# Kernel tuning notes

Hardware: AMD Instinct MI355X
Metric: run time of the kernel (lower is better)

Reference implementation:

```python
import jax, jax.numpy as jnp
import numpy as np

EPS = 1e-12
NEG_SLOPE = 0.2

def _normalize(x):
    # F.normalize(x, p=2, dim=1)
    n = jnp.sqrt(jnp.sum(x * x, axis=-1, keepdims=True))
    return x / jnp.maximum(n, EPS)

def setup_inputs() -> dict:
    key = jax.random.key(0)
    ks = jax.random.split(key, 10)
    n_users, n_items, n_entities = 100000, 50000, 200000
    n_rel, n_edges, n_inter, n_hops, d = 32, 2000000, 1000000, 2, 64
    return {
        "user_emb": jax.random.normal(ks[0], (n_users, d), jnp.float32) * 0.1,
        "entity_emb": jax.random.normal(ks[1], (n_entities, d), jnp.float32) * 0.1,
        "rel_weight": jax.random.normal(ks[2], (n_rel, d), jnp.float32) * 0.1,
        "gate1_w": jax.random.normal(ks[3], (n_hops, d, d), jnp.float32) * 0.1,
        "gate2_w": jax.random.normal(ks[4], (n_hops, d, d), jnp.float32) * 0.1,
        "head": jax.random.randint(ks[5], (n_edges,), 0, n_entities, jnp.int32),
        "tail": jax.random.randint(ks[6], (n_edges,), 0, n_entities, jnp.int32),
        "edge_type": jax.random.randint(ks[7], (n_edges,), 0, n_rel, jnp.int32),
        "mat_row": jax.random.randint(ks[8], (n_inter,), 0, n_users, jnp.int32),
        "mat_col": jax.random.randint(ks[9], (n_inter,), 0, n_items, jnp.int32),
    }

def reference(user_emb, entity_emb, rel_weight, gate1_w, gate2_w,
              head, tail, edge_type, mat_row, mat_col):
    n_users = user_emb.shape[0]
    n_entities = entity_emb.shape[0]
    n_items = 50000
    n_hops = gate1_w.shape[0]

    entity_res = entity_emb
    user_res = user_emb
    for i in range(n_hops):
        # KG aggregate: gather-scale-scatter over KG triples
        msg = entity_emb[tail] * rel_weight[edge_type]          # [E, d]
        entity_agg = jax.ops.segment_sum(msg, head, num_segments=n_entities)
        # CF aggregate: user -> item
        item_neigh = user_emb[mat_row] * rel_weight[0]          # [I, d]
        i_u_agg = jax.ops.segment_sum(item_neigh, mat_col, num_segments=n_items)
        # gated fusion of KG-side and CF-side item embeddings
        ea_items = entity_agg[:n_items]
        gi = jax.nn.leaky_relu(ea_items @ gate1_w[i].T + i_u_agg @ gate2_w[i].T,
                               negative_slope=NEG_SLOPE)
        item_fusion = gi * ea_items + (1.0 - gi) * i_u_agg
        # sparse mm with binary user-item matrix == segment_sum over rows
        user_agg = jax.ops.segment_sum(item_fusion[mat_col], mat_row,
                                       num_segments=n_users)
        entity_emb = jnp.concatenate([item_fusion, entity_agg[n_items:]], axis=0)
        entity_emb = _normalize(entity_emb)
        user_emb = _normalize(user_agg)
        entity_res = entity_res + entity_emb
        user_res = user_res + user_emb
    # concatenate outputs: [n_entities + n_users, d]
    return jnp.concatenate([entity_res, user_res], axis=0)
```

## Files before the change

kernel.cpp:

```cpp
#include <hip/hip_runtime.h>
#include <hip/hip_bf16.h>

#define D 64
#define N_USERS 100000
#define N_ITEMS 50000
#define N_ENT   200000
#define EPS 1e-12f
#define CHUNK 4096
#define NBINP 512
#define CAP   8192

typedef unsigned short u16;
typedef unsigned int u32;
typedef unsigned long long u64;

template<int MODE> struct Cfg;
template<> struct Cfg<0> { static constexpr int SHIFT = 9; static constexpr int NSEG = N_ENT;   };
template<> struct Cfg<1> { static constexpr int SHIFT = 7; static constexpr int NSEG = N_ITEMS; };
template<> struct Cfg<2> { static constexpr int SHIFT = 8; static constexpr int NSEG = N_USERS; };
template<int MODE> constexpr int nbin_of() {
  return (Cfg<MODE>::NSEG + (1 << Cfg<MODE>::SHIFT) - 1) >> Cfg<MODE>::SHIFT;
}

__device__ __forceinline__ float bf2f(u16 u) {
  return __uint_as_float(((unsigned)u) << 16);
}
__device__ __forceinline__ u16 f2bf(float f) {
  unsigned u = __float_as_uint(f);
  unsigned r = (u + 0x7FFFu + ((u >> 16) & 1u)) >> 16;
  return (u16)r;
}
__device__ __forceinline__ float wave_rsqnorm(float v) {
  float ss = v * v;
#pragma unroll
  for (int m = 1; m < 64; m <<= 1) ss += __shfl_xor(ss, m);
  return 1.f / fmaxf(sqrtf(ss), EPS);
}
__device__ __forceinline__ float bcast(float v, int k) {
  return __uint_as_float(__builtin_amdgcn_readlane(__float_as_uint(v), k));
}

__global__ __launch_bounds__(256) void init_embed(
    const float* __restrict__ ent, const float* __restrict__ usr,
    float* __restrict__ out_ent, float* __restrict__ out_usr,
    u16* __restrict__ ent_bf, u16* __restrict__ usr_bf) {
  int i = blockIdx.x * 256 + threadIdx.x;
  if (i < N_ENT * D) {
    float v = ent[i];
    out_ent[i] = v;
    ent_bf[i] = f2bf(v);
  }
  if (i < N_USERS * D) {
    float v = usr[i];
    out_usr[i] = v;
    usr_bf[i] = f2bf(v);
  }
}

__global__ __launch_bounds__(256) void scan_block(
    const int* __restrict__ in, int* __restrict__ out,
    int* __restrict__ bsum, int n) {
  __shared__ int sm[256];
  int tid = threadIdx.x;
  int i = blockIdx.x * 256 + tid;
  int v = (i < n) ? in[i] : 0;
  sm[tid] = v;
  __syncthreads();
  for (int ofs = 1; ofs < 256; ofs <<= 1) {
    int t = (tid >= ofs) ? sm[tid - ofs] : 0;
    __syncthreads();
    sm[tid] += t;
    __syncthreads();
  }
  if (i < n) out[i] = sm[tid] - v;
  if (tid == 255) bsum[blockIdx.x] = sm[255];
}

__global__ __launch_bounds__(1024) void scan_top(int* __restrict__ bsum, int nb) {
  __shared__ int sm[1024];
  int tid = threadIdx.x;
  int v = (tid < nb) ? bsum[tid] : 0;
  sm[tid] = v;
  __syncthreads();
  for (int ofs = 1; ofs < 1024; ofs <<= 1) {
    int t = (tid >= ofs) ? sm[tid - ofs] : 0;
    __syncthreads();
    sm[tid] += t;
    __syncthreads();
  }
  if (tid < nb) bsum[tid] = sm[tid] - v;
}

__global__ __launch_bounds__(256) void scan_addv(
    int* __restrict__ out, const int* __restrict__ bsum, int n) {
  int i = blockIdx.x * 256 + threadIdx.x;
  if (i < n) out[i] += bsum[blockIdx.x];
}

template<int MODE>
__global__ __launch_bounds__(256) void p1_hist(
    const int* __restrict__ keys, int n, int* __restrict__ bc, int nblk) {
  constexpr int SHIFT = Cfg<MODE>::SHIFT;
  constexpr int NBIN = nbin_of<MODE>();
  __shared__ int h[NBINP];
  int tid = threadIdx.x;
  h[tid] = 0; h[tid + 256] = 0;
  __syncthreads();
  int base = blockIdx.x * CHUNK;
  int end = min(base + CHUNK, n);
  for (int i = base + tid; i < end; i += 256)
    atomicAdd(&h[keys[i] >> SHIFT], 1);
  __syncthreads();
  for (int b = tid; b < NBIN; b += 256)
    bc[b * nblk + blockIdx.x] = h[b];
}

template<int MODE>
__global__ __launch_bounds__(256) void p1_scatter(
    const int* __restrict__ keys, const int* __restrict__ pa,
    const int* __restrict__ pb, int n, const int* __restrict__ sbc, int nblk,
    int2* __restrict__ out) {
  constexpr int SHIFT = Cfg<MODE>::SHIFT;
  constexpr int NBIN = nbin_of<MODE>();
  __shared__ int h[NBINP];
  __shared__ int cur[NBINP];
  __shared__ int bb[NBINP];
  __shared__ int2 staged[CHUNK];
  __shared__ int dstA[CHUNK];
  int tid = threadIdx.x;
  h[tid] = 0; h[tid + 256] = 0;
  __syncthreads();
  int base = blockIdx.x * CHUNK;
  int end = min(base + CHUNK, n);
  for (int i = base + tid; i < end; i += 256)
    atomicAdd(&h[keys[i] >> SHIFT], 1);
  __syncthreads();
  int o0 = h[tid], o1 = h[tid + 256];
  for (int ofs = 1; ofs < NBINP; ofs <<= 1) {
    int v0 = (tid >= ofs) ? h[tid - ofs] : 0;
    int v1 = (tid + 256 >= ofs) ? h[tid + 256 - ofs] : 0;
    __syncthreads();
    h[tid] += v0; h[tid + 256] += v1;
    __syncthreads();
  }
  int e0 = h[tid] - o0, e1 = h[tid + 256] - o1;
  cur[tid] = e0; cur[tid + 256] = e1;
  if (tid < NBIN)        bb[tid] = sbc[tid * nblk + blockIdx.x] - e0;
  if (tid + 256 < NBIN)  bb[tid + 256] = sbc[(tid + 256) * nblk + blockIdx.x] - e1;
  __syncthreads();
  for (int i = base + tid; i < end; i += 256) {
    int k = keys[i];
    int bin = k >> SHIFT;
    int payload;
    if constexpr (MODE == 0) payload = pa[i] | (pb[i] << 24);
    else                     payload = pa[i];
    int lp = atomicAdd(&cur[bin], 1);
    staged[lp] = make_int2(k, payload);
    dstA[lp] = bb[bin] + lp;
  }
  __syncthreads();
  int cnt = end - base;
  for (int t = tid; t < cnt; t += 256) out[dstA[t]] = staged[t];
}

template<int MODE>
__global__ __launch_bounds__(256) void p2_sort(
    const int2* __restrict__ binned, const int* __restrict__ sbc, int nblk,
    int n, int* __restrict__ vals, int* __restrict__ hids,
    int* __restrict__ off) {
  constexpr int SHIFT = Cfg<MODE>::SHIFT;
  constexpr int NSEG = Cfg<MODE>::NSEG;
  constexpr int SEGBIN = 1 << SHIFT;
  constexpr int NBIN = nbin_of<MODE>();
  __shared__ int h[NBINP];
  __shared__ int cur[NBINP];
  __shared__ int staged[CAP];
  int tid = threadIdx.x;
  int b = blockIdx.x;
  int start = sbc[b * nblk];
  int endp = (b == NBIN - 1) ? n : sbc[(b + 1) * nblk];
  int cnt = endp - start;
  h[tid] = 0; h[tid + 256] = 0;
  __syncthreads();
  int segbase = b << SHIFT;
  for (int t = tid; t < cnt; t += 256)
    atomicAdd(&h[binned[start + t].x - segbase], 1);
  __syncthreads();
  int o0 = h[tid], o1 = h[tid + 256];
  for (int ofs = 1; ofs < NBINP; ofs <<= 1) {
    int v0 = (tid >= ofs) ? h[tid - ofs] : 0;
    int v1 = (tid + 256 >= ofs) ? h[tid + 256 - ofs] : 0;
    __syncthreads();
    h[tid] += v0; h[tid + 256] += v1;
    __syncthreads();
  }
  int e0 = h[tid] - o0, e1 = h[tid + 256] - o1;
  if (tid < SEGBIN && segbase + tid < NSEG) off[segbase + tid] = start + e0;
  if (tid + 256 < SEGBIN && segbase + tid + 256 < NSEG)
    off[segbase + tid + 256] = start + e1;
  if (b == NBIN - 1 && tid == 0) off[NSEG] = n;
  cur[tid] = e0; cur[tid + 256] = e1;
  __syncthreads();
  if (cnt <= CAP) {
    for (int t = tid; t < cnt; t += 256) {
      int2 e = binned[start + t];
      int lp = atomicAdd(&cur[e.x - segbase], 1);
      staged[lp] = e.y;
      hids[start + lp] = e.x;
    }
    __syncthreads();
    for (int t = tid; t < cnt; t += 256) vals[start + t] = staged[t];
  } else {
    for (int t = tid; t < cnt; t += 256) {
      int2 e = binned[start + t];
      int lp = atomicAdd(&cur[e.x - segbase], 1);
      vals[start + lp] = e.y;
      hids[start + lp] = e.x;
    }
  }
}

template<bool REL>
__global__ __launch_bounds__(256) void edge_gather(
    const u16* __restrict__ tab, const float* __restrict__ relw,
    const int* __restrict__ pk, const int* __restrict__ hid,
    float* __restrict__ raw, int n) {
  __shared__ float lds_relw[REL ? 32 * D : 1];
  if (REL) {
    for (int i = threadIdx.x; i < 32 * D; i += 256) lds_relw[i] = relw[i];
    __syncthreads();
  }
  int win = blockIdx.x * 4 + (threadIdx.x >> 6);
  int S = win * 64;
  if (S >= n) return;
  int lane = threadIdx.x & 63;
  int cnt = min(64, n - S);
  int p  = (S + lane < n) ? pk[S + lane]  : 0;
  int hd = (S + lane < n) ? hid[S + lane] : -3;
  int hp = (S > 0) ? hid[S - 1] : -4;
  int hn = (S + 64 < n) ? hid[S + 64] : -5;
  int hnl = __shfl_down(hd, 1);
  if (lane == 63) hnl = hn;
  u64 real = __ballot(hd != hnl);
  if (cnt < 64) real &= (1ull << cnt) - 1ull;
  u64 emit = real | (1ull << (cnt - 1));
  bool start_in = (__shfl(hd, 0) != hp);
  float acc = 0.f;
  if (cnt == 64) {
    for (int base = 0; base < 64; base += 8) {
      u16 r[8]; int et[8];
#pragma unroll
      for (int k = 0; k < 8; ++k) {
        int q = __shfl(p, base + k);
        if (REL) {
          r[k] = tab[(size_t)(q & 0xFFFFFF) * D + lane];
          et[k] = ((unsigned)q) >> 24;
        } else {
          r[k] = tab[(size_t)q * D + lane];
        }
      }
#pragma unroll
      for (int k = 0; k < 8; ++k) {
        int j = base + k;
        float c = bf2f(r[k]);
        if (REL) c *= lds_relw[et[k] * D + lane];
        acc += c;
        if ((emit >> j) & 1ull) {
          int h = __shfl(hd, j);
          float* dst = raw + (size_t)h * D + lane;
          if (start_in && ((real >> j) & 1ull)) *dst = acc;
          else atomicAdd(dst, acc);
          acc = 0.f;
          start_in = true;
        }
      }
    }
  } else {
    for (int j = 0; j < cnt; ++j) {
      int q = __shfl(p, j);
      float c;
      if (REL) c = bf2f(tab[(size_t)(q & 0xFFFFFF) * D + lane]) *
                   lds_relw[(((unsigned)q) >> 24) * D + lane];
      else     c = bf2f(tab[(size_t)q * D + lane]);
      acc += c;
      if ((emit >> j) & 1ull) {
        int h = __shfl(hd, j);
        float* dst = raw + (size_t)h * D + lane;
        if (start_in && ((real >> j) & 1ull)) *dst = acc;
        else atomicAdd(dst, acc);
        acc = 0.f;
        start_in = true;
      }
    }
  }
}

__global__ __launch_bounds__(256) void fin_rows(
    const float* __restrict__ raw, u16* __restrict__ out_bf,
    float* __restrict__ res, int row0, int nrows) {
  int r = blockIdx.x * 4 + (threadIdx.x >> 6);
  if (r >= nrows) return;
  int row = row0 + r;
  int lane = threadIdx.x & 63;
  size_t o = (size_t)row * D + lane;
  float v = raw[o];
  float nv = v * wave_rsqnorm(v);
  out_bf[o] = f2bf(nv);
  res[o] += nv;
}

__global__ __launch_bounds__(256) void fuse_items(
    const float* __restrict__ ent_raw, const float* __restrict__ iu,
    const float* __restrict__ relw,
    const float* __restrict__ g1, const float* __restrict__ g2,
    u16* __restrict__ fus_bf, u16* __restrict__ ent_bf,
    float* __restrict__ res) {
  __shared__ float G1[D][D + 1];
  __shared__ float G2[D][D + 1];
  for (int i = threadIdx.x; i < D * D; i += 256) {
    G1[i >> 6][i & 63] = g1[i];
    G2[i >> 6][i & 63] = g2[i];
  }
  __syncthreads();
  int row = blockIdx.x * 4 + (threadIdx.x >> 6);
  if (row >= N_ITEMS) return;
  int lane = threadIdx.x & 63;
  size_t o = (size_t)row * D + lane;
  float eav = ent_raw[o];
  float uv = iu[o] * relw[lane];
  float s1 = 0.f, s2 = 0.f;
#pragma unroll
  for (int k = 0; k < D; ++k) {
    s1 += bcast(eav, k) * G1[lane][k];
    s2 += bcast(uv, k) * G2[lane][k];
  }
  float s = s1 + s2;
  float gi = s > 0.f ? s : 0.2f * s;
  float fus = gi * eav + (1.f - gi) * uv;
  fus_bf[o] = f2bf(fus);
  float nv = fus * wave_rsqnorm(fus);
  ent_bf[o] = f2bf(nv);
  res[o] += nv;
}

template<int MODE>
static void run_sort(const int* keys, const int* pa, const int* pb, int n,
                     int2* binned, int* vals, int* hids, int* off, int* bc,
                     int* bsum, hipStream_t stream) {
  constexpr int NBIN = nbin_of<MODE>();
  int nblk = (n + CHUNK - 1) / CHUNK;
  int len = NBIN * nblk;
  p1_hist<MODE><<<nblk, 256, 0, stream>>>(keys, n, bc, nblk);
  int nbs = (len + 255) / 256;
  scan_block<<<nbs, 256, 0, stream>>>(bc, bc, bsum, len);
  scan_top<<<1, 1024, 0, stream>>>(bsum, nbs);
  scan_addv<<<nbs, 256, 0, stream>>>(bc, bsum, len);
  p1_scatter<MODE><<<nblk, 256, 0, stream>>>(keys, pa, pb, n, bc, nblk, binned);
  p2_sort<MODE><<<NBIN, 256, 0, stream>>>(binned, bc, nblk, n, vals, hids, off);
}

extern "C" void kernel_launch(void* const* d_in, const int* in_sizes, int n_in,
                              void* d_out, int out_size, void* d_ws, size_t ws_size,
                              hipStream_t stream) {
  const float* user_emb = (const float*)d_in[0];
  const float* ent_emb  = (const float*)d_in[1];
  const float* relw     = (const float*)d_in[2];
  const float* g1       = (const float*)d_in[3];
  const float* g2       = (const float*)d_in[4];
  const int*   head     = (const int*)d_in[5];
  const int*   tail     = (const int*)d_in[6];
  const int*   etype    = (const int*)d_in[7];
  const int*   mrow     = (const int*)d_in[8];
  const int*   mcol     = (const int*)d_in[9];

  const int n_edges = in_sizes[5];
  const int n_inter = in_sizes[8];
  const int n_hops  = in_sizes[3] / (D * D);

  u16* ent_bf = (u16*)d_ws;
  u16* usr_bf = ent_bf + (size_t)N_ENT * D;
  u16* fus_bf = usr_bf + (size_t)N_USERS * D;
  float* ent_raw = (float*)(fus_bf + (size_t)N_ITEMS * D);
  float* usr_raw = ent_raw + (size_t)N_ENT * D;
  float* iu      = usr_raw;
  int* ip = (int*)(usr_raw + (size_t)N_USERS * D);
  int* o_head = ip;   ip += N_ENT + 1;
  int* o_col  = ip;   ip += N_ITEMS + 1;
  int* o_row  = ip;   ip += N_USERS + 1;
  int* pk_head = ip;  ip += n_edges;
  int* hid_h   = ip;  ip += n_edges;
  int* vr_col  = ip;  ip += n_inter;
  int* hid_c   = ip;  ip += n_inter;
  int* vc_row  = ip;  ip += n_inter;
  int* hid_r   = ip;  ip += n_inter;
  int* bc      = ip;  ip += 391 * ((n_edges + CHUNK - 1) / CHUNK) + 64;
  int* bsum    = ip;  ip += 1024;

  float* out_ent = (float*)d_out;
  float* out_usr = out_ent + (size_t)N_ENT * D;

  int2* bin_head = (int2*)d_out;
  int2* bin_col  = bin_head + n_edges;
  int2* bin_row  = bin_col + n_inter;

  run_sort<0>(head, tail, etype, n_edges, bin_head, pk_head, hid_h, o_head,
              bc, bsum, stream);
  run_sort<1>(mcol, mrow, nullptr, n_inter, bin_col, vr_col, hid_c, o_col,
              bc, bsum, stream);
  run_sort<2>(mrow, mcol, nullptr, n_inter, bin_row, vc_row, hid_r, o_row,
              bc, bsum, stream);

  init_embed<<<(N_ENT * D + 255) / 256, 256, 0, stream>>>(
      ent_emb, user_emb, out_ent, out_usr, ent_bf, usr_bf);

  const int nwin_kg = (n_edges + 63) / 64;
  const int nwin_in = (n_inter + 63) / 64;

  for (int i = 0; i < n_hops; ++i) {
    hipMemsetAsync(ent_raw, 0, (size_t)N_ENT * D * sizeof(float), stream);
    hipMemsetAsync(iu, 0, (size_t)N_ITEMS * D * sizeof(float), stream);

    edge_gather<true><<<(nwin_kg + 3) / 4, 256, 0, stream>>>(
        ent_bf, relw, pk_head, hid_h, ent_raw, n_edges);

    edge_gather<false><<<(nwin_in + 3) / 4, 256, 0, stream>>>(
        usr_bf, nullptr, vr_col, hid_c, iu, n_inter);

    fuse_items<<<(N_ITEMS + 3) / 4, 256, 0, stream>>>(
        ent_raw, iu, relw, g1 + (size_t)i * D * D, g2 + (size_t)i * D * D,
        fus_bf, ent_bf, out_ent);

    fin_rows<<<(N_ENT - N_ITEMS + 3) / 4, 256, 0, stream>>>(
        ent_raw, ent_bf, out_ent, N_ITEMS, N_ENT - N_ITEMS);

    hipMemsetAsync(usr_raw, 0, (size_t)N_USERS * D * sizeof(float), stream);
    edge_gather<false><<<(nwin_in + 3) / 4, 256, 0, stream>>>(
        fus_bf, nullptr, vc_row, hid_r, usr_raw, n_inter);

    fin_rows<<<(N_USERS + 3) / 4, 256, 0, stream>>>(
        usr_raw, usr_bf, out_usr, 0, N_USERS);
  }
}
```

Baseline: 588.8 us.

## Streamline sort binning and defer residual accumulation to one final pass

The preprocessing sort now builds global bin totals with atomics and has each block claim its bin slots atomically. This replaces the per-block histogram matrix and its three-kernel scan, and drops the segment offset writes. The item-fusion and entity-normalize kernels are merged into one launch, and the two per-hop memsets become one. The per-hop fp32 residual read-modify-write is removed: each hop's normalized embeddings go to ping-pong bf16 tables, and a single final_combine kernel sums them with the original fp32 inputs. The trade-off is that the residual terms are now summed from bf16-rounded values, and the order of elements within each bin depends on atomic timing.

```diff
diff --git a/kernel.cpp b/kernel.cpp
--- a/kernel.cpp
+++ b/kernel.cpp
@@ -7,6 +7,8 @@
 #define N_ENT   200000
 #define EPS 1e-12f
 #define CHUNK 4096
+#define HCHUNK 16384
+#define NBIN  391
 #define NBINP 512
 #define CAP   8192
 
@@ -18,9 +20,6 @@
 template<> struct Cfg<0> { static constexpr int SHIFT = 9; static constexpr int NSEG = N_ENT;   };
 template<> struct Cfg<1> { static constexpr int SHIFT = 7; static constexpr int NSEG = N_ITEMS; };
 template<> struct Cfg<2> { static constexpr int SHIFT = 8; static constexpr int NSEG = N_USERS; };
-template<int MODE> constexpr int nbin_of() {
-  return (Cfg<MODE>::NSEG + (1 << Cfg<MODE>::SHIFT) - 1) >> Cfg<MODE>::SHIFT;
-}
 
 __device__ __forceinline__ float bf2f(u16 u) {
   return __uint_as_float(((unsigned)u) << 16);
@@ -40,145 +39,104 @@
   return __uint_as_float(__builtin_amdgcn_readlane(__float_as_uint(v), k));
 }
 
-__global__ __launch_bounds__(256) void init_embed(
+__global__ __launch_bounds__(256) void conv_embed(
     const float* __restrict__ ent, const float* __restrict__ usr,
-    float* __restrict__ out_ent, float* __restrict__ out_usr,
     u16* __restrict__ ent_bf, u16* __restrict__ usr_bf) {
   int i = blockIdx.x * 256 + threadIdx.x;
-  if (i < N_ENT * D) {
-    float v = ent[i];
-    out_ent[i] = v;
-    ent_bf[i] = f2bf(v);
-  }
-  if (i < N_USERS * D) {
-    float v = usr[i];
-    out_usr[i] = v;
-    usr_bf[i] = f2bf(v);
-  }
-}
-
-__global__ __launch_bounds__(256) void scan_block(
-    const int* __restrict__ in, int* __restrict__ out,
-    int* __restrict__ bsum, int n) {
-  __shared__ int sm[256];
-  int tid = threadIdx.x;
-  int i = blockIdx.x * 256 + tid;
-  int v = (i < n) ? in[i] : 0;
-  sm[tid] = v;
-  __syncthreads();
-  for (int ofs = 1; ofs < 256; ofs <<= 1) {
-    int t = (tid >= ofs) ? sm[tid - ofs] : 0;
-    __syncthreads();
-    sm[tid] += t;
-    __syncthreads();
-  }
-  if (i < n) out[i] = sm[tid] - v;
-  if (tid == 255) bsum[blockIdx.x] = sm[255];
-}
-
-__global__ __launch_bounds__(1024) void scan_top(int* __restrict__ bsum, int nb) {
-  __shared__ int sm[1024];
-  int tid = threadIdx.x;
-  int v = (tid < nb) ? bsum[tid] : 0;
-  sm[tid] = v;
-  __syncthreads();
-  for (int ofs = 1; ofs < 1024; ofs <<= 1) {
-    int t = (tid >= ofs) ? sm[tid - ofs] : 0;
-    __syncthreads();
-    sm[tid] += t;
-    __syncthreads();
-  }
-  if (tid < nb) bsum[tid] = sm[tid] - v;
-}
-
-__global__ __launch_bounds__(256) void scan_addv(
-    int* __restrict__ out, const int* __restrict__ bsum, int n) {
-  int i = blockIdx.x * 256 + threadIdx.x;
-  if (i < n) out[i] += bsum[blockIdx.x];
-}
-
-template<int MODE>
-__global__ __launch_bounds__(256) void p1_hist(
-    const int* __restrict__ keys, int n, int* __restrict__ bc, int nblk) {
-  constexpr int SHIFT = Cfg<MODE>::SHIFT;
-  constexpr int NBIN = nbin_of<MODE>();
+  if (i < N_ENT * D) ent_bf[i] = f2bf(ent[i]);
+  if (i < N_USERS * D) usr_bf[i] = f2bf(usr[i]);
+}
+
+__global__ __launch_bounds__(256) void hist_tot(
+    const int* __restrict__ keys, int n, int shift, int* __restrict__ tot) {
   __shared__ int h[NBINP];
   int tid = threadIdx.x;
   h[tid] = 0; h[tid + 256] = 0;
   __syncthreads();
+  int base = blockIdx.x * HCHUNK;
+  int end = min(base + HCHUNK, n);
+  for (int i = base + tid; i < end; i += 256)
+    atomicAdd(&h[keys[i] >> shift], 1);
+  __syncthreads();
+  for (int b = tid; b < NBIN; b += 256)
+    if (h[b]) atomicAdd(&tot[b], h[b]);
+}
+
+__global__ __launch_bounds__(512) void scan_bases(
+    const int* __restrict__ tot, int* __restrict__ bases,
+    int* __restrict__ cur, int n0, int n1, int n2) {
+  __shared__ int sm[512];
+  int tid = threadIdx.x;
+  for (int s = 0; s < 3; ++s) {
+    int tn = (s == 0) ? n0 : ((s == 1) ? n1 : n2);
+    int v = (tid < NBIN) ? tot[s * 392 + tid] : 0;
+    __syncthreads();
+    sm[tid] = v;
+    __syncthreads();
+    for (int ofs = 1; ofs < 512; ofs <<= 1) {
+      int t = (tid >= ofs) ? sm[tid - ofs] : 0;
+      __syncthreads();
+      sm[tid] += t;
+      __syncthreads();
+    }
+    if (tid < NBIN) {
+      int b = sm[tid] - v;
+      bases[s * 392 + tid] = b;
+      cur[s * 392 + tid] = b;
+    }
+    if (tid == 0) bases[s * 392 + NBIN] = tn;
+  }
+}
+
+template<int MODE>
+__global__ __launch_bounds__(256) void p1_direct(
+    const int* __restrict__ keys, const int* __restrict__ pa,
+    const int* __restrict__ pb, int n, int* __restrict__ cur,
+    int2* __restrict__ out) {
+  constexpr int SHIFT = Cfg<MODE>::SHIFT;
+  __shared__ int lkeys[CHUNK];
+  __shared__ int h[NBINP];
+  __shared__ int bb[NBINP];
+  __shared__ int lcur[NBINP];
+  int tid = threadIdx.x;
+  h[tid] = 0; h[tid + 256] = 0;
+  __syncthreads();
   int base = blockIdx.x * CHUNK;
   int end = min(base + CHUNK, n);
-  for (int i = base + tid; i < end; i += 256)
-    atomicAdd(&h[keys[i] >> SHIFT], 1);
-  __syncthreads();
-  for (int b = tid; b < NBIN; b += 256)
-    bc[b * nblk + blockIdx.x] = h[b];
-}
-
-template<int MODE>
-__global__ __launch_bounds__(256) void p1_scatter(
-    const int* __restrict__ keys, const int* __restrict__ pa,
-    const int* __restrict__ pb, int n, const int* __restrict__ sbc, int nblk,
-    int2* __restrict__ out) {
-  constexpr int SHIFT = Cfg<MODE>::SHIFT;
-  constexpr int NBIN = nbin_of<MODE>();
-  __shared__ int h[NBINP];
-  __shared__ int cur[NBINP];
-  __shared__ int bb[NBINP];
-  __shared__ int2 staged[CHUNK];
-  __shared__ int dstA[CHUNK];
-  int tid = threadIdx.x;
-  h[tid] = 0; h[tid + 256] = 0;
-  __syncthreads();
-  int base = blockIdx.x * CHUNK;
-  int end = min(base + CHUNK, n);
-  for (int i = base + tid; i < end; i += 256)
-    atomicAdd(&h[keys[i] >> SHIFT], 1);
-  __syncthreads();
-  int o0 = h[tid], o1 = h[tid + 256];
-  for (int ofs = 1; ofs < NBINP; ofs <<= 1) {
-    int v0 = (tid >= ofs) ? h[tid - ofs] : 0;
-    int v1 = (tid + 256 >= ofs) ? h[tid + 256 - ofs] : 0;
-    __syncthreads();
-    h[tid] += v0; h[tid + 256] += v1;
-    __syncthreads();
-  }
-  int e0 = h[tid] - o0, e1 = h[tid + 256] - o1;
-  cur[tid] = e0; cur[tid + 256] = e1;
-  if (tid < NBIN)        bb[tid] = sbc[tid * nblk + blockIdx.x] - e0;
-  if (tid + 256 < NBIN)  bb[tid + 256] = sbc[(tid + 256) * nblk + blockIdx.x] - e1;
-  __syncthreads();
   for (int i = base + tid; i < end; i += 256) {
     int k = keys[i];
-    int bin = k >> SHIFT;
+    lkeys[i - base] = k;
+    atomicAdd(&h[k >> SHIFT], 1);
+  }
+  __syncthreads();
+  for (int b = tid; b < NBINP; b += 256) {
+    lcur[b] = 0;
+    if (b < NBIN && h[b] > 0) bb[b] = atomicAdd(&cur[b], h[b]);
+  }
+  __syncthreads();
+  for (int i = base + tid; i < end; i += 256) {
+    int k = lkeys[i - base];
     int payload;
     if constexpr (MODE == 0) payload = pa[i] | (pb[i] << 24);
     else                     payload = pa[i];
-    int lp = atomicAdd(&cur[bin], 1);
-    staged[lp] = make_int2(k, payload);
-    dstA[lp] = bb[bin] + lp;
-  }
-  __syncthreads();
-  int cnt = end - base;
-  for (int t = tid; t < cnt; t += 256) out[dstA[t]] = staged[t];
+    int bin = k >> SHIFT;
+    int lp = atomicAdd(&lcur[bin], 1);
+    out[bb[bin] + lp] = make_int2(k, payload);
+  }
 }
 
 template<int MODE>
 __global__ __launch_bounds__(256) void p2_sort(
-    const int2* __restrict__ binned, const int* __restrict__ sbc, int nblk,
-    int n, int* __restrict__ vals, int* __restrict__ hids,
-    int* __restrict__ off) {
+    const int2* __restrict__ binned, const int* __restrict__ bases,
+    int* __restrict__ vals, int* __restrict__ hids) {
   constexpr int SHIFT = Cfg<MODE>::SHIFT;
-  constexpr int NSEG = Cfg<MODE>::NSEG;
-  constexpr int SEGBIN = 1 << SHIFT;
-  constexpr int NBIN = nbin_of<MODE>();
   __shared__ int h[NBINP];
   __shared__ int cur[NBINP];
   __shared__ int staged[CAP];
   int tid = threadIdx.x;
   int b = blockIdx.x;
-  int start = sbc[b * nblk];
-  int endp = (b == NBIN - 1) ? n : sbc[(b + 1) * nblk];
+  int start = bases[b];
+  int endp = bases[b + 1];
   int cnt = endp - start;
   h[tid] = 0; h[tid + 256] = 0;
   __syncthreads();
@@ -195,10 +153,6 @@
     __syncthreads();
   }
   int e0 = h[tid] - o0, e1 = h[tid + 256] - o1;
-  if (tid < SEGBIN && segbase + tid < NSEG) off[segbase + tid] = start + e0;
-  if (tid + 256 < SEGBIN && segbase + tid + 256 < NSEG)
-    off[segbase + tid + 256] = start + e1;
-  if (b == NBIN - 1 && tid == 0) off[NSEG] = n;
   cur[tid] = e0; cur[tid + 256] = e1;
   __syncthreads();
   if (cnt <= CAP) {
@@ -295,68 +249,73 @@
   }
 }
 
-__global__ __launch_bounds__(256) void fin_rows(
-    const float* __restrict__ raw, u16* __restrict__ out_bf,
-    float* __restrict__ res, int row0, int nrows) {
-  int r = blockIdx.x * 4 + (threadIdx.x >> 6);
-  if (r >= nrows) return;
-  int row = row0 + r;
+__global__ __launch_bounds__(256) void finalize_entities(
+    const float* __restrict__ ent_raw, const float* __restrict__ iu,
+    const float* __restrict__ relw, const float* __restrict__ g1,
+    const float* __restrict__ g2, u16* __restrict__ fus_bf,
+    u16* __restrict__ ent_out) {
+  __shared__ float G1[D][D + 1];
+  __shared__ float G2[D][D + 1];
+  if (blockIdx.x * 4 < N_ITEMS) {
+    for (int i = threadIdx.x; i < D * D; i += 256) {
+      G1[i >> 6][i & 63] = g1[i];
+      G2[i >> 6][i & 63] = g2[i];
+    }
+    __syncthreads();
+  }
+  int row = blockIdx.x * 4 + (threadIdx.x >> 6);
+  if (row >= N_ENT) return;
   int lane = threadIdx.x & 63;
   size_t o = (size_t)row * D + lane;
+  if (row < N_ITEMS) {
+    float eav = ent_raw[o];
+    float uv = iu[o] * relw[lane];
+    float s1 = 0.f, s2 = 0.f;
+#pragma unroll
+    for (int k = 0; k < D; ++k) {
+      s1 += bcast(eav, k) * G1[lane][k];
+      s2 += bcast(uv, k) * G2[lane][k];
+    }
+    float s = s1 + s2;
+    float gi = s > 0.f ? s : 0.2f * s;
+    float fus = gi * eav + (1.f - gi) * uv;
+    fus_bf[o] = f2bf(fus);
+    float nv = fus * wave_rsqnorm(fus);
+    ent_out[o] = f2bf(nv);
+  } else {
+    float v = ent_raw[o];
+    float nv = v * wave_rsqnorm(v);
+    ent_out[o] = f2bf(nv);
+  }
+}
+
+__global__ __launch_bounds__(256) void fin_users(
+    const float* __restrict__ raw, u16* __restrict__ out_bf) {
+  int r = blockIdx.x * 4 + (threadIdx.x >> 6);
+  if (r >= N_USERS) return;
+  int lane = threadIdx.x & 63;
+  size_t o = (size_t)r * D + lane;
   float v = raw[o];
   float nv = v * wave_rsqnorm(v);
   out_bf[o] = f2bf(nv);
-  res[o] += nv;
-}
-
-__global__ __launch_bounds__(256) void fuse_items(
-    const float* __restrict__ ent_raw, const float* __restrict__ iu,
-    const float* __restrict__ relw,
-    const float* __restrict__ g1, const float* __restrict__ g2,
-    u16* __restrict__ fus_bf, u16* __restrict__ ent_bf,
-    float* __restrict__ res) {
-  __shared__ float G1[D][D + 1];
-  __shared__ float G2[D][D + 1];
-  for (int i = threadIdx.x; i < D * D; i += 256) {
-    G1[i >> 6][i & 63] = g1[i];
-    G2[i >> 6][i & 63] = g2[i];
-  }
-  __syncthreads();
-  int row = blockIdx.x * 4 + (threadIdx.x >> 6);
-  if (row >= N_ITEMS) return;
-  int lane = threadIdx.x & 63;
-  size_t o = (size_t)row * D + lane;
-  float eav = ent_raw[o];
-  float uv = iu[o] * relw[lane];
-  float s1 = 0.f, s2 = 0.f;
-#pragma unroll
-  for (int k = 0; k < D; ++k) {
-    s1 += bcast(eav, k) * G1[lane][k];
-    s2 += bcast(uv, k) * G2[lane][k];
-  }
-  float s = s1 + s2;
-  float gi = s > 0.f ? s : 0.2f * s;
-  float fus = gi * eav + (1.f - gi) * uv;
-  fus_bf[o] = f2bf(fus);
-  float nv = fus * wave_rsqnorm(fus);
-  ent_bf[o] = f2bf(nv);
-  res[o] += nv;
-}
-
-template<int MODE>
-static void run_sort(const int* keys, const int* pa, const int* pb, int n,
-                     int2* binned, int* vals, int* hids, int* off, int* bc,
-                     int* bsum, hipStream_t stream) {
-  constexpr int NBIN = nbin_of<MODE>();
-  int nblk = (n + CHUNK - 1) / CHUNK;
-  int len = NBIN * nblk;
-  p1_hist<MODE><<<nblk, 256, 0, stream>>>(keys, n, bc, nblk);
-  int nbs = (len + 255) / 256;
-  scan_block<<<nbs, 256, 0, stream>>>(bc, bc, bsum, len);
-  scan_top<<<1, 1024, 0, stream>>>(bsum, nbs);
-  scan_addv<<<nbs, 256, 0, stream>>>(bc, bsum, len);
-  p1_scatter<MODE><<<nblk, 256, 0, stream>>>(keys, pa, pb, n, bc, nblk, binned);
-  p2_sort<MODE><<<NBIN, 256, 0, stream>>>(binned, bc, nblk, n, vals, hids, off);
+}
+
+__global__ __launch_bounds__(256) void final_combine(
+    const float* __restrict__ ent0, const float* __restrict__ usr0,
+    const u16* __restrict__ e1, const u16* __restrict__ e2,
+    const u16* __restrict__ u1, const u16* __restrict__ u2,
+    float* __restrict__ out_ent, float* __restrict__ out_usr, int two) {
+  int i = blockIdx.x * 256 + threadIdx.x;
+  if (i < N_ENT * D) {
+    float v = ent0[i] + bf2f(e1[i]);
+    if (two) v += bf2f(e2[i]);
+    out_ent[i] = v;
+  }
+  if (i < N_USERS * D) {
+    float v = usr0[i] + bf2f(u1[i]);
+    if (two) v += bf2f(u2[i]);
+    out_usr[i] = v;
+  }
 }
 
 extern "C" void kernel_launch(void* const* d_in, const int* in_sizes, int n_in,
@@ -377,67 +336,88 @@
   const int n_inter = in_sizes[8];
   const int n_hops  = in_sizes[3] / (D * D);
 
-  u16* ent_bf = (u16*)d_ws;
-  u16* usr_bf = ent_bf + (size_t)N_ENT * D;
-  u16* fus_bf = usr_bf + (size_t)N_USERS * D;
-  float* ent_raw = (float*)(fus_bf + (size_t)N_ITEMS * D);
-  float* usr_raw = ent_raw + (size_t)N_ENT * D;
-  float* iu      = usr_raw;
+  u16* entA = (u16*)d_ws;
+  u16* entB = entA + (size_t)N_ENT * D;
+  u16* usrA = entB + (size_t)N_ENT * D;
+  u16* usrB = usrA + (size_t)N_USERS * D;
+  u16* fus_bf = usrB + (size_t)N_USERS * D;
+  float* usr_raw = (float*)(fus_bf + (size_t)N_ITEMS * D);
   int* ip = (int*)(usr_raw + (size_t)N_USERS * D);
-  int* o_head = ip;   ip += N_ENT + 1;
-  int* o_col  = ip;   ip += N_ITEMS + 1;
-  int* o_row  = ip;   ip += N_USERS + 1;
   int* pk_head = ip;  ip += n_edges;
   int* hid_h   = ip;  ip += n_edges;
   int* vr_col  = ip;  ip += n_inter;
   int* hid_c   = ip;  ip += n_inter;
   int* vc_row  = ip;  ip += n_inter;
   int* hid_r   = ip;  ip += n_inter;
-  int* bc      = ip;  ip += 391 * ((n_edges + CHUNK - 1) / CHUNK) + 64;
-  int* bsum    = ip;  ip += 1024;
-
-  float* out_ent = (float*)d_out;
-  float* out_usr = out_ent + (size_t)N_ENT * D;
-
+  int* tot     = ip;  ip += 392 * 3;
+  int* bases   = ip;  ip += 392 * 3;
+  int* cur     = ip;  ip += 392 * 3;
+
+  float* ent_raw = (float*)d_out;
+  float* iu      = ent_raw + (size_t)N_ENT * D;
   int2* bin_head = (int2*)d_out;
   int2* bin_col  = bin_head + n_edges;
   int2* bin_row  = bin_col + n_inter;
-
-  run_sort<0>(head, tail, etype, n_edges, bin_head, pk_head, hid_h, o_head,
-              bc, bsum, stream);
-  run_sort<1>(mcol, mrow, nullptr, n_inter, bin_col, vr_col, hid_c, o_col,
-              bc, bsum, stream);
-  run_sort<2>(mrow, mcol, nullptr, n_inter, bin_row, vc_row, hid_r, o_row,
-              bc, bsum, stream);
-
-  init_embed<<<(N_ENT * D + 255) / 256, 256, 0, stream>>>(
-      ent_emb, user_emb, out_ent, out_usr, ent_bf, usr_bf);
+  float* out_ent = (float*)d_out;
+  float* out_usr = out_ent + (size_t)N_ENT * D;
+
+  hipMemsetAsync(tot, 0, 392 * 3 * sizeof(int), stream);
+  hist_tot<<<(n_edges + HCHUNK - 1) / HCHUNK, 256, 0, stream>>>(
+      head, n_edges, 9, tot);
+  hist_tot<<<(n_inter + HCHUNK - 1) / HCHUNK, 256, 0, stream>>>(
+      mcol, n_inter, 7, tot + 392);
+  hist_tot<<<(n_inter + HCHUNK - 1) / HCHUNK, 256, 0, stream>>>(
+      mrow, n_inter, 8, tot + 784);
+  scan_bases<<<1, 512, 0, stream>>>(tot, bases, cur, n_edges, n_inter, n_inter);
+
+  p1_direct<0><<<(n_edges + CHUNK - 1) / CHUNK, 256, 0, stream>>>(
+      head, tail, etype, n_edges, cur, bin_head);
+  p1_direct<1><<<(n_inter + CHUNK - 1) / CHUNK, 256, 0, stream>>>(
+      mcol, mrow, nullptr, n_inter, cur + 392, bin_col);
+  p1_direct<2><<<(n_inter + CHUNK - 1) / CHUNK, 256, 0, stream>>>(
+      mrow, mcol, nullptr, n_inter, cur + 784, bin_row);
+
+  p2_sort<0><<<NBIN, 256, 0, stream>>>(bin_head, bases, pk_head, hid_h);
+  p2_sort<1><<<NBIN, 256, 0, stream>>>(bin_col, bases + 392, vr_col, hid_c);
+  p2_sort<2><<<NBIN, 256, 0, stream>>>(bin_row, bases + 784, vc_row, hid_r);
+
+  conv_embed<<<(N_ENT * D + 255) / 256, 256, 0, stream>>>(
+      ent_emb, user_emb, entA, usrA);
 
   const int nwin_kg = (n_edges + 63) / 64;
   const int nwin_in = (n_inter + 63) / 64;
+  u16* etab[2] = {entA, entB};
+  u16* utab[2] = {usrA, usrB};
 
   for (int i = 0; i < n_hops; ++i) {
-    hipMemsetAsync(ent_raw, 0, (size_t)N_ENT * D * sizeof(float), stream);
-    hipMemsetAsync(iu, 0, (size_t)N_ITEMS * D * sizeof(float), stream);
+    const u16* ein = etab[i & 1];
+    u16* eout      = etab[(i + 1) & 1];
+    const u16* uin = utab[i & 1];
+    u16* uout      = utab[(i + 1) & 1];
+
+    hipMemsetAsync(ent_raw, 0,
+                   (size_t)(N_ENT + N_ITEMS) * D * sizeof(float), stream);
 
     edge_gather<true><<<(nwin_kg + 3) / 4, 256, 0, stream>>>(
-        ent_bf, relw, pk_head, hid_h, ent_raw, n_edges);
-
+        ein, relw, pk_head, hid_h, ent_raw, n_edges);
     edge_gather<false><<<(nwin_in + 3) / 4, 256, 0, stream>>>(
-        usr_bf, nullptr, vr_col, hid_c, iu, n_inter);
-
-    fuse_items<<<(N_ITEMS + 3) / 4, 256, 0, stream>>>(
+        uin, nullptr, vr_col, hid_c, iu, n_inter);
+
+    finalize_entities<<<(N_ENT + 3) / 4, 256, 0, stream>>>(
         ent_raw, iu, relw, g1 + (size_t)i * D * D, g2 + (size_t)i * D * D,
-        fus_bf, ent_bf, out_ent);
-
-    fin_rows<<<(N_ENT - N_ITEMS + 3) / 4, 256, 0, stream>>>(
-        ent_raw, ent_bf, out_ent, N_ITEMS, N_ENT - N_ITEMS);
+        fus_bf, eout);
 
     hipMemsetAsync(usr_raw, 0, (size_t)N_USERS * D * sizeof(float), stream);
     edge_gather<false><<<(nwin_in + 3) / 4, 256, 0, stream>>>(
         fus_bf, nullptr, vc_row, hid_r, usr_raw, n_inter);
-
-    fin_rows<<<(N_USERS + 3) / 4, 256, 0, stream>>>(
-        usr_raw, usr_bf, out_usr, 0, N_USERS);
-  }
-}
+    fin_users<<<(N_USERS + 3) / 4, 256, 0, stream>>>(usr_raw, uout);
+  }
+
+  const u16* e1 = etab[1];
+  const u16* u1 = utab[1];
+  const u16* e2 = (n_hops >= 2) ? etab[0] : etab[1];
+  const u16* u2 = (n_hops >= 2) ? utab[0] : utab[1];
+  final_combine<<<(N_ENT * D + 255) / 256, 256, 0, stream>>>(
+      ent_emb, user_emb, e1, e2, u1, u2, out_ent, out_usr,
+      (n_hops >= 2) ? 1 : 0);
+}
```

Result: slower. 705.4 us (+19.8%).
